# Optimization experiments

Hardware: AMD Instinct MI355X
Metric: run time of the kernel (lower is better)

Reference implementation:

```python
import jax, jax.numpy as jnp
import numpy as np

EMBED_DIM = 1024
NUM_HEADS = 16
HEAD_DIM = EMBED_DIM // NUM_HEADS
SCALING = HEAD_DIM ** -0.5


def setup_inputs() -> dict:
    key = jax.random.key(0)
    ks = jax.random.split(key, 10)
    T, B, E = 2048, 2, EMBED_DIM
    s = 0.02
    return {
        "query": jax.random.normal(ks[0], (T, B, E), jnp.float32),
        "key_padding_mask": jnp.zeros((B, T), jnp.bool_),
        "attn_mask": jnp.zeros((T, T), jnp.float32),
        "Wq": jax.random.normal(ks[1], (E, E), jnp.float32) * s,
        "bq": jnp.zeros((E,), jnp.float32),
        "Wk": jax.random.normal(ks[2], (E, E), jnp.float32) * s,
        "bk": jnp.zeros((E,), jnp.float32),
        "Wv": jax.random.normal(ks[3], (E, E), jnp.float32) * s,
        "bv": jnp.zeros((E,), jnp.float32),
        "Wo": jax.random.normal(ks[4], (E, E), jnp.float32) * s,
        "bo": jnp.zeros((E,), jnp.float32),
    }


def reference(query, key_padding_mask, attn_mask, Wq, bq, Wk, bk, Wv, bv, Wo, bo):
    T, B, E = query.shape
    H, D = NUM_HEADS, HEAD_DIM
    # projections (nn.Linear: x @ W.T + b)
    q = (query @ Wq.T + bq) * SCALING
    k_new = query @ Wk.T + bk  # returned as new_keys
    v_new = query @ Wv.T + bv  # returned as new_values
    S = T  # self-attention, no cache
    # [T, B, E] -> [B*H, T, D]
    qh = q.reshape(T, B * H, D).transpose(1, 0, 2)
    kh = k_new.reshape(S, B * H, D).transpose(1, 0, 2)
    vh = v_new.reshape(S, B * H, D).transpose(1, 0, 2)
    # scores: [B*H, T, S]
    scores = jnp.einsum("btd,bsd->bts", qh, kh)
    scores = scores + attn_mask[None, :, :]
    # key padding mask: [B, S] -> broadcast over heads / tgt
    scores = scores.reshape(B, H, T, S)
    scores = jnp.where(key_padding_mask[:, None, None, :], -jnp.inf, scores)
    scores = scores.reshape(B * H, T, S)
    attn_weights = jax.nn.softmax(scores.astype(jnp.float32), axis=-1)
    attn_probs = attn_weights.astype(query.dtype)  # dropout p=0.0
    out = jnp.einsum("bts,bsd->btd", attn_probs, vh)  # [B*H, T, D]
    out = out.transpose(1, 0, 2).reshape(T, B, E)
    attn_output = out @ Wo.T + bo
    return (attn_output, attn_weights.reshape(B, H, T, S), k_new, v_new)
```

## Files before the change

kernel.cpp:

```cpp
#include <hip/hip_runtime.h>
#include <hip/hip_bf16.h>
#include <stdint.h>

typedef __bf16 bf16_t;
typedef __bf16 bf16x8 __attribute__((ext_vector_type(8)));
typedef float f32x4 __attribute__((ext_vector_type(4)));

#define SCALING 0.125f
#define EXPBIAS 20.0f

#define WS_XQ  (0u)
#define WS_W   (8u << 20)
#define WS_QH  (16u << 20)
#define WS_KH  (24u << 20)
#define WS_VT  (32u << 20)
#define WS_X2  (40u << 20)
#define WS_AM  (48u << 20)

#define OFF_OUT 0
#define OFF_WEI 4194304
#define OFF_K   138412032
#define OFF_V   142606336

typedef const __attribute__((address_space(1))) void gvoid_t;
typedef __attribute__((address_space(3))) void lvoid_t;

__device__ inline void gload_lds16(const void* g, void* l) {
  __builtin_amdgcn_global_load_lds((gvoid_t*)g, (lvoid_t*)l, 16, 0, 0);
}

__global__ __launch_bounds__(256) void prep_kernel(
    const float* __restrict__ q,
    const float* __restrict__ w0, const float* __restrict__ w1,
    const float* __restrict__ w2, const float* __restrict__ w3,
    const float* __restrict__ am,
    bf16_t* __restrict__ Xq, bf16_t* __restrict__ Wbf, float* __restrict__ af) {
  const int blk = blockIdx.x;
  const int tid = threadIdx.x;
  if (blk < 4096) {
    int i = blk * 256 + tid;
    float4 v = ((const float4*)q)[i];
    union { bf16_t h[4]; uint2 u; } o;
    o.h[0] = (bf16_t)v.x; o.h[1] = (bf16_t)v.y;
    o.h[2] = (bf16_t)v.z; o.h[3] = (bf16_t)v.w;
    ((uint2*)Xq)[i] = o.u;
  } else if (blk < 8192) {
    int i = (blk - 4096) * 256 + tid;
    int wsel = i >> 18;
    int loc = i & 262143;
    const float* src = (wsel == 0) ? w0 : (wsel == 1) ? w1 : (wsel == 2) ? w2 : w3;
    float4 v = ((const float4*)src)[loc];
    union { bf16_t h[4]; uint2 u; } o;
    o.h[0] = (bf16_t)v.x; o.h[1] = (bf16_t)v.y;
    o.h[2] = (bf16_t)v.z; o.h[3] = (bf16_t)v.w;
    ((uint2*)(Wbf + (size_t)wsel * 1048576))[loc] = o.u;
  } else {
    int o = (blk - 8192) * 256 + tid;
    int lane = o & 63;
    int f = o >> 6;
    int st = f & 15;
    int wslab = (f >> 4) & 7;
    int tt = f >> 7;
    int t = tt * 16 + (lane & 15);
    int s = wslab * 256 + 32 * (st >> 1) + 4 * (st & 1) + 8 * (lane >> 4);
    float4 v = *(const float4*)&am[(size_t)t * 2048 + s];
    v.x -= EXPBIAS; v.y -= EXPBIAS; v.z -= EXPBIAS; v.w -= EXPBIAS;
    *(float4*)&af[(size_t)o * 4] = v;
  }
}

#define CSTRIDE 134
__global__ __launch_bounds__(256) void gemm_nt(
    const bf16_t* __restrict__ Xq, const bf16_t* __restrict__ X2,
    const bf16_t* __restrict__ Wall,
    const float* __restrict__ bq, const float* __restrict__ bk,
    const float* __restrict__ bv, const float* __restrict__ bo,
    float* __restrict__ dout,
    bf16_t* __restrict__ qh, bf16_t* __restrict__ kh, bf16_t* __restrict__ vT,
    int mode_base) {
  const int mode = mode_base + blockIdx.z;
  const bf16_t* __restrict__ X = (mode < 3) ? Xq : X2;
  const bf16_t* __restrict__ W = Wall + (size_t)mode * 1048576;
  const float* __restrict__ bias = (mode == 0) ? bq : (mode == 1) ? bk : (mode == 2) ? bv : bo;

  const int hwid = blockIdx.y * 8 + blockIdx.x;
  const int tile = (hwid & 7) * 32 + (hwid >> 3);
  const int bx = tile & 7, by = tile >> 3;

  __shared__ alignas(16) bf16_t SM[128 * CSTRIDE];
  bf16_t* Alds = SM;
  bf16_t* Blds = SM + 8192;

  const int lane = threadIdx.x & 63;
  const int w = threadIdx.x >> 6;
  const int wr = w >> 1, wc = w & 1;
  const int m0 = by * 128, n0 = bx * 128;

  f32x4 acc[4][4] = {};

  for (int kk = 0; kk < 1024; kk += 64) {
    __syncthreads();
    const int rb = w * 32;
#pragma unroll
    for (int i = 0; i < 4; ++i) {
      int r = rb + i * 8 + (lane >> 3);
      int c = (lane & 7) * 8;
      gload_lds16(X + (size_t)(m0 + r) * 1024 + kk + c, &Alds[(rb + i * 8) * 64]);
      gload_lds16(W + (size_t)(n0 + r) * 1024 + kk + c, &Blds[(rb + i * 8) * 64]);
    }
    __syncthreads();
#pragma unroll
    for (int kx = 0; kx < 2; ++kx) {
      bf16x8 af[4], bfr[4];
#pragma unroll
      for (int mi = 0; mi < 4; ++mi)
        af[mi] = *(const bf16x8*)&Alds[(wr * 64 + mi * 16 + (lane & 15)) * 64 + kx * 32 + (lane >> 4) * 8];
#pragma unroll
      for (int ni = 0; ni < 4; ++ni)
        bfr[ni] = *(const bf16x8*)&Blds[(wc * 64 + ni * 16 + (lane & 15)) * 64 + kx * 32 + (lane >> 4) * 8];
#pragma unroll
      for (int mi = 0; mi < 4; ++mi)
#pragma unroll
        for (int ni = 0; ni < 4; ++ni)
          acc[mi][ni] = __builtin_amdgcn_mfma_f32_16x16x32_bf16(af[mi], bfr[ni], acc[mi][ni], 0, 0, 0);
    }
  }

  if (mode == 1 || mode == 2) {
    __syncthreads();
#pragma unroll
    for (int mi = 0; mi < 4; ++mi) {
#pragma unroll
      for (int ni = 0; ni < 4; ++ni) {
#pragma unroll
        for (int r = 0; r < 4; ++r) {
          int il = wr * 64 + mi * 16 + (lane >> 4) * 4 + r;
          int jl = wc * 64 + ni * 16 + (lane & 15);
          float v = acc[mi][ni][r] + bias[n0 + jl];
          dout[(mode == 1 ? OFF_K : OFF_V) + (size_t)(m0 + il) * 1024 + n0 + jl] = v;
          SM[il * CSTRIDE + jl] = (bf16_t)v;
        }
      }
    }
    __syncthreads();
    const int s0 = m0 >> 1;
    const int b_ = w >> 1;
    const int hl = w & 1;
    const int bh = b_ * 16 + (n0 >> 6) + hl;
    if (mode == 1) {
      bf16_t* dst = kh + (size_t)bh * 131072;
#pragma unroll
      for (int f = 0; f < 8; ++f) {
        int sbl = f >> 2, par = (f >> 1) & 1, dh = f & 1;
        int il = 2 * (sbl * 32 + ((lane >> 2) & 3) * 8 + par * 4 + (lane & 3)) + b_;
        int jl = hl * 64 + dh * 32 + (lane >> 4) * 8;
        bf16x8 fr = *(const bf16x8*)&SM[il * CSTRIDE + jl];
        int fi = ((s0 >> 5) + sbl) * 4 + par * 2 + dh;
        *(bf16x8*)&dst[(size_t)fi * 512 + lane * 8] = fr;
      }
    } else {
      bf16_t* dst = vT + (size_t)bh * 131072;
#pragma unroll
      for (int f = 0; f < 8; ++f) {
        int sbl = f >> 2, dq = f & 3;
        int jl = hl * 64 + dq * 16 + (lane & 15);
        int il0 = 2 * (sbl * 32 + (lane >> 4) * 8) + b_;
        bf16x8 fr;
#pragma unroll
        for (int e = 0; e < 8; ++e) fr[e] = SM[(il0 + 2 * e) * CSTRIDE + jl];
        int fi = ((s0 >> 5) + sbl) * 4 + dq;
        *(bf16x8*)&dst[(size_t)fi * 512 + lane * 8] = fr;
      }
    }
  } else {
#pragma unroll
    for (int mi = 0; mi < 4; ++mi) {
#pragma unroll
      for (int ni = 0; ni < 4; ++ni) {
#pragma unroll
        for (int r = 0; r < 4; ++r) {
          int i = m0 + wr * 64 + mi * 16 + (lane >> 4) * 4 + r;
          int j = n0 + wc * 64 + ni * 16 + (lane & 15);
          float v = acc[mi][ni][r] + bias[j];
          int t = i >> 1, b = i & 1, h = j >> 6, d = j & 63;
          int bh = b * 16 + h;
          if (mode == 0) {
            qh[(size_t)bh * 131072 + t * 64 + d] = (bf16_t)(v * SCALING);
          } else {
            dout[OFF_OUT + (size_t)i * 1024 + j] = v;
          }
        }
      }
    }
  }
}

#define ALOAD(n, K0, K1, MV, KU)                                                   \
  {                                                                                \
    const int fi_ = (w * 8 + ((n) >> 1)) * 4 + ((n) & 1) * 2;                      \
    K0 = *(const bf16x8*)&kfrag[(size_t)fi_ * 512 + lane * 8];                     \
    K1 = *(const bf16x8*)&kfrag[(size_t)(fi_ + 1) * 512 + lane * 8];               \
    MV = *(const float4*)&afrag[(n) * 256 + lane * 4];                             \
    KU = *(const uint32_t*)&kpm[b * 2048 + s0w + 32 * ((n) >> 1) + 4 * ((n) & 1) + 8 * g]; \
  }

__global__ __launch_bounds__(512, 4) void attn_kernel(
    const bf16_t* __restrict__ qh, const bf16_t* __restrict__ kh,
    const bf16_t* __restrict__ vT,
    const float* __restrict__ amaskF, const uint8_t* __restrict__ kpm,
    float* __restrict__ wout, bf16_t* __restrict__ X2) {
  const int lane = threadIdx.x & 63;
  const int w = threadIdx.x >> 6;
  const int lt = lane & 15;
  const int g = lane >> 4;
  const int bh = blockIdx.x;
  const int tt = blockIdx.y;
  const int t0 = tt * 16;
  const int b = bh >> 4;

  __shared__ float wsum[16][8];
  __shared__ float pbuf[8][16][68];
  __shared__ float sbuf[8][16][33];

  const bf16_t* __restrict__ qbase = qh + (size_t)bh * 131072;
  const bf16_t* __restrict__ kfrag = kh + (size_t)bh * 131072;
  const bf16_t* __restrict__ vfrag = vT + (size_t)bh * 131072;
  const float* __restrict__ afrag = amaskF + ((size_t)(tt * 8 + w) * 16) * 256;
  float* __restrict__ wrow = wout + (size_t)bh * 4194304;
  const int s0w = w * 256;

  bf16x8 aq[2];
#pragma unroll
  for (int kx = 0; kx < 2; ++kx)
    aq[kx] = *(const bf16x8*)&qbase[(t0 + lt) * 64 + kx * 32 + g * 8];

  bf16x8 pa[8];
  float ssum = 0.f;

  bf16x8 ka0, ka1, kb0, kb1, kc0, kc1;
  float4 ma, mb, mc;
  uint32_t ua, ub, uc;
  ALOAD(0, ka0, ka1, ma, ua);
  ALOAD(1, kb0, kb1, mb, ub);
#pragma unroll
  for (int st = 0; st < 16; ++st) {
    if (st < 14) {
      ALOAD(st + 2, kc0, kc1, mc, uc);
    }
    f32x4 acc = {0.f, 0.f, 0.f, 0.f};
    acc = __builtin_amdgcn_mfma_f32_16x16x32_bf16(ka0, aq[0], acc, 0, 0, 0);
    acc = __builtin_amdgcn_mfma_f32_16x16x32_bf16(ka1, aq[1], acc, 0, 0, 0);
#pragma unroll
    for (int r = 0; r < 4; ++r) {
      float m = (r == 0) ? ma.x : (r == 1) ? ma.y : (r == 2) ? ma.z : ma.w;
      float val = acc[r] + m;
      val = ((ua >> (8 * r)) & 0xff) ? -__builtin_inff() : val;
      float e = __expf(val);
      ssum += e;
      pa[st >> 1][4 * (st & 1) + r] = (bf16_t)e;
    }
    ka0 = kb0; ka1 = kb1; ma = mb; ua = ub;
    kb0 = kc0; kb1 = kc1; mb = mc; ub = uc;
  }

  ssum += __shfl_xor(ssum, 16, 64);
  ssum += __shfl_xor(ssum, 32, 64);
  if (lane < 16) wsum[lane][w] = ssum;
  __syncthreads();
  float ss = 0.f;
#pragma unroll
  for (int ww = 0; ww < 8; ++ww) ss += wsum[lt][ww];
  const float rl = 1.0f / ss;

  f32x4 po[4] = {};
  bf16x8 vfa[4], vfb[4];
#pragma unroll
  for (int dt = 0; dt < 4; ++dt)
    vfa[dt] = *(const bf16x8*)&vfrag[(size_t)((w * 8) * 4 + dt) * 512 + lane * 8];
#pragma unroll
  for (int kx = 0; kx < 8; ++kx) {
    if (kx < 7) {
#pragma unroll
      for (int dt = 0; dt < 4; ++dt)
        vfb[dt] = *(const bf16x8*)&vfrag[(size_t)((w * 8 + kx + 1) * 4 + dt) * 512 + lane * 8];
    }
    f32x4 wv0, wv1;
#pragma unroll
    for (int r = 0; r < 4; ++r) { wv0[r] = (float)pa[kx][r] * rl; wv1[r] = (float)pa[kx][4 + r] * rl; }
    *(f32x4*)&sbuf[w][lt][8 * g] = wv0;
    *(f32x4*)&sbuf[w][lt][8 * g + 4] = wv1;
    __builtin_amdgcn_s_setprio(1);
#pragma unroll
    for (int dt = 0; dt < 4; ++dt)
      po[dt] = __builtin_amdgcn_mfma_f32_16x16x32_bf16(vfa[dt], pa[kx], po[dt], 0, 0, 0);
    __builtin_amdgcn_s_setprio(0);
    asm volatile("s_waitcnt lgkmcnt(0)" ::: "memory");
#pragma unroll
    for (int p = 0; p < 2; ++p) {
      int row = 8 * p + (lane >> 3);
      int c4 = (lane & 7) * 4;
      f32x4 rv = *(const f32x4*)&sbuf[w][row][c4];
      __builtin_nontemporal_store(rv,
          (f32x4*)&wrow[(size_t)(t0 + row) * 2048 + s0w + 32 * kx + c4]);
    }
#pragma unroll
    for (int dt = 0; dt < 4; ++dt) vfa[dt] = vfb[dt];
  }
#pragma unroll
  for (int dt = 0; dt < 4; ++dt) po[dt] *= rl;

#pragma unroll
  for (int dt = 0; dt < 4; ++dt) {
    f32x4 v = po[dt];
    *(f32x4*)&pbuf[w][lt][dt * 16 + 4 * g] = v;
  }
  __syncthreads();
  int e0 = threadIdx.x * 2;
  int row = e0 >> 6, d = e0 & 63;
  float v0 = 0.f, v1 = 0.f;
#pragma unroll
  for (int ww = 0; ww < 8; ++ww) {
    v0 += pbuf[ww][row][d];
    v1 += pbuf[ww][row][d + 1];
  }
  int h = bh & 15;
  union { bf16_t hh[2]; uint32_t u; } pk;
  pk.hh[0] = (bf16_t)v0; pk.hh[1] = (bf16_t)v1;
  *(uint32_t*)&X2[(size_t)((t0 + row) * 2 + b) * 1024 + h * 64 + d] = pk.u;
}

extern "C" void kernel_launch(void* const* d_in, const int* in_sizes, int n_in,
                              void* d_out, int out_size, void* d_ws, size_t ws_size,
                              hipStream_t stream) {
  (void)in_sizes; (void)n_in; (void)out_size; (void)ws_size;
  const float* query = (const float*)d_in[0];
  const uint8_t* kpm = (const uint8_t*)d_in[1];
  const float* amask = (const float*)d_in[2];
  const float* Wq = (const float*)d_in[3];
  const float* bq = (const float*)d_in[4];
  const float* Wk = (const float*)d_in[5];
  const float* bk = (const float*)d_in[6];
  const float* Wv = (const float*)d_in[7];
  const float* bv = (const float*)d_in[8];
  const float* Wo = (const float*)d_in[9];
  const float* bo = (const float*)d_in[10];
  float* dout = (float*)d_out;
  char* ws = (char*)d_ws;

  bf16_t* Xq = (bf16_t*)(ws + WS_XQ);
  bf16_t* Wbf = (bf16_t*)(ws + WS_W);
  bf16_t* qh = (bf16_t*)(ws + WS_QH);
  bf16_t* kh = (bf16_t*)(ws + WS_KH);
  bf16_t* vT = (bf16_t*)(ws + WS_VT);
  bf16_t* X2 = (bf16_t*)(ws + WS_X2);
  float* amF = (float*)(ws + WS_AM);

  prep_kernel<<<12288, 256, 0, stream>>>(query, Wq, Wk, Wv, Wo, amask, Xq, Wbf, amF);
  gemm_nt<<<dim3(8, 32, 3), 256, 0, stream>>>(Xq, X2, Wbf, bq, bk, bv, bo, dout, qh, kh, vT, 0);
  attn_kernel<<<dim3(32, 128), 512, 0, stream>>>(qh, kh, vT, amF, kpm, dout + OFF_WEI, X2);
  gemm_nt<<<dim3(8, 32, 1), 256, 0, stream>>>(Xq, X2, Wbf, bq, bk, bv, bo, dout, qh, kh, vT, 3);
}
```

Measured before the change: 242.9 us.

## Double-buffer LDS tiles in projection GEMM with prefetch of next K-slice

Replaces the single-buffered 64-wide K loop with a double-buffered 32-wide K loop. The next slice's global-to-LDS loads are issued before computing on the current buffer, and each iteration now needs one barrier instead of two. This aims to hide global load latency behind MFMA work, at the cost of twice as many iterations. The LDS row stride drops to 32, which may change bank-conflict behaviour.

```diff
diff --git a/kernel.cpp b/kernel.cpp
--- a/kernel.cpp
+++ b/kernel.cpp
@@ -88,46 +88,58 @@
   const int bx = tile & 7, by = tile >> 3;
 
   __shared__ alignas(16) bf16_t SM[128 * CSTRIDE];
-  bf16_t* Alds = SM;
-  bf16_t* Blds = SM + 8192;
 
   const int lane = threadIdx.x & 63;
   const int w = threadIdx.x >> 6;
   const int wr = w >> 1, wc = w & 1;
   const int m0 = by * 128, n0 = bx * 128;
 
+  const int srow = (lane >> 2);
+  const int scol = (lane & 3) * 8;
+
   f32x4 acc[4][4] = {};
 
-  for (int kk = 0; kk < 1024; kk += 64) {
+#pragma unroll
+  for (int p = 0; p < 2; ++p) {
+    gload_lds16(X + (size_t)(m0 + p * 64 + w * 16 + srow) * 1024 + 0 + scol,
+                &SM[0 + (p * 4 + w) * 512]);
+    gload_lds16(W + (size_t)(n0 + p * 64 + w * 16 + srow) * 1024 + 0 + scol,
+                &SM[8192 + (p * 4 + w) * 512]);
+  }
+  __syncthreads();
+
+  int cur = 0;
+  for (int t = 0; t < 32; ++t) {
+    if (t < 31) {
+      const int kk = (t + 1) * 32;
+      const int nxt = cur ^ 1;
+#pragma unroll
+      for (int p = 0; p < 2; ++p) {
+        gload_lds16(X + (size_t)(m0 + p * 64 + w * 16 + srow) * 1024 + kk + scol,
+                    &SM[nxt * 4096 + (p * 4 + w) * 512]);
+        gload_lds16(W + (size_t)(n0 + p * 64 + w * 16 + srow) * 1024 + kk + scol,
+                    &SM[8192 + nxt * 4096 + (p * 4 + w) * 512]);
+      }
+    }
+    const bf16_t* Ab = &SM[cur * 4096];
+    const bf16_t* Bb = &SM[8192 + cur * 4096];
+    bf16x8 af[4], bfr[4];
+#pragma unroll
+    for (int mi = 0; mi < 4; ++mi)
+      af[mi] = *(const bf16x8*)&Ab[(wr * 64 + mi * 16 + (lane & 15)) * 32 + (lane >> 4) * 8];
+#pragma unroll
+    for (int ni = 0; ni < 4; ++ni)
+      bfr[ni] = *(const bf16x8*)&Bb[(wc * 64 + ni * 16 + (lane & 15)) * 32 + (lane >> 4) * 8];
+#pragma unroll
+    for (int mi = 0; mi < 4; ++mi)
+#pragma unroll
+      for (int ni = 0; ni < 4; ++ni)
+        acc[mi][ni] = __builtin_amdgcn_mfma_f32_16x16x32_bf16(af[mi], bfr[ni], acc[mi][ni], 0, 0, 0);
     __syncthreads();
-    const int rb = w * 32;
-#pragma unroll
-    for (int i = 0; i < 4; ++i) {
-      int r = rb + i * 8 + (lane >> 3);
-      int c = (lane & 7) * 8;
-      gload_lds16(X + (size_t)(m0 + r) * 1024 + kk + c, &Alds[(rb + i * 8) * 64]);
-      gload_lds16(W + (size_t)(n0 + r) * 1024 + kk + c, &Blds[(rb + i * 8) * 64]);
-    }
-    __syncthreads();
-#pragma unroll
-    for (int kx = 0; kx < 2; ++kx) {
-      bf16x8 af[4], bfr[4];
-#pragma unroll
-      for (int mi = 0; mi < 4; ++mi)
-        af[mi] = *(const bf16x8*)&Alds[(wr * 64 + mi * 16 + (lane & 15)) * 64 + kx * 32 + (lane >> 4) * 8];
-#pragma unroll
-      for (int ni = 0; ni < 4; ++ni)
-        bfr[ni] = *(const bf16x8*)&Blds[(wc * 64 + ni * 16 + (lane & 15)) * 64 + kx * 32 + (lane >> 4) * 8];
-#pragma unroll
-      for (int mi = 0; mi < 4; ++mi)
-#pragma unroll
-        for (int ni = 0; ni < 4; ++ni)
-          acc[mi][ni] = __builtin_amdgcn_mfma_f32_16x16x32_bf16(af[mi], bfr[ni], acc[mi][ni], 0, 0, 0);
-    }
+    cur ^= 1;
   }
 
   if (mode == 1 || mode == 2) {
-    __syncthreads();
 #pragma unroll
     for (int mi = 0; mi < 4; ++mi) {
 #pragma unroll
```

New measurement: 240.3 us. About the same (-1.1%).
